# Kernel tuning notes

Hardware: AMD Instinct MI355X
Metric: run time of the kernel (lower is better)

Reference implementation:

```python
import jax, jax.numpy as jnp
import numpy as np
from jax import lax

B, L, W, C, H = 2, 64, 64, 128, 4
DH = C // H  # 32
SCALE = 32 ** -0.5  # dim_head ** -0.5
BN_EPS = 1e-3  # keras BatchNormalization default epsilon


def _sep_conv(x, dwk, dwb, g, b, mu, var, pwk, pwb):
    # Depthwise 3x3 conv, 'same' padding (NHWC, kernel HWIO with groups=C)
    y = lax.conv_general_dilated(
        x, dwk, window_strides=(1, 1), padding='SAME',
        dimension_numbers=('NHWC', 'HWIO', 'NHWC'),
        feature_group_count=x.shape[-1]) + dwb
    # BatchNorm (inference mode: moving statistics)
    y = g * (y - mu) * lax.rsqrt(var + BN_EPS) + b
    # Pointwise 1x1 conv
    return jnp.einsum('blwc,cf->blwf', y, pwk) + pwb


def setup_inputs() -> dict:
    key = jax.random.key(0)
    ks = jax.random.split(key, 32)
    d = {'x': jax.random.normal(ks[0], (B, L * W, C), dtype=jnp.float32)}
    i = 1
    for p in ('q', 'k', 'v'):
        d[p + '_dwk'] = jax.random.normal(ks[i], (3, 3, 1, C), jnp.float32) * 0.1; i += 1
        d[p + '_dwb'] = jax.random.normal(ks[i], (C,), jnp.float32) * 0.05; i += 1
        d[p + '_g'] = jnp.ones((C,), jnp.float32) + jax.random.normal(ks[i], (C,), jnp.float32) * 0.05; i += 1
        d[p + '_b'] = jax.random.normal(ks[i], (C,), jnp.float32) * 0.05; i += 1
        d[p + '_mu'] = jax.random.normal(ks[i], (C,), jnp.float32) * 0.05; i += 1
        d[p + '_var'] = jnp.abs(jax.random.normal(ks[i], (C,), jnp.float32) * 0.1) + 0.9; i += 1
        d[p + '_pwk'] = jax.random.normal(ks[i], (C, C), jnp.float32) * (C ** -0.5); i += 1
        d[p + '_pwb'] = jax.random.normal(ks[i], (C,), jnp.float32) * 0.05; i += 1
    d['out_w'] = jax.random.normal(ks[i], (C, C), jnp.float32) * (C ** -0.5); i += 1
    d['out_b'] = jax.random.normal(ks[i], (C,), jnp.float32) * 0.05
    return d


def reference(x,
              q_dwk, q_dwb, q_g, q_b, q_mu, q_var, q_pwk, q_pwb,
              k_dwk, k_dwb, k_g, k_b, k_mu, k_var, k_pwk, k_pwb,
              v_dwk, v_dwb, v_g, v_b, v_mu, v_var, v_pwk, v_pwb,
              out_w, out_b):
    xi = x.reshape(B, L, W, C)  # 'b (l w) c -> b l w c'
    def heads(t):  # 'b l w (h d) -> b h (l w) d'
        return t.reshape(B, L * W, H, DH).transpose(0, 2, 1, 3)
    q = heads(_sep_conv(xi, q_dwk, q_dwb, q_g, q_b, q_mu, q_var, q_pwk, q_pwb))
    k = heads(_sep_conv(xi, k_dwk, k_dwb, k_g, k_b, k_mu, k_var, k_pwk, k_pwb))
    v = heads(_sep_conv(xi, v_dwk, v_dwb, v_g, v_b, v_mu, v_var, v_pwk, v_pwb))
    dots = jnp.einsum('bhid,bhjd->bhij', q, k) * SCALE
    attn = jax.nn.softmax(dots, axis=-1)
    out = jnp.einsum('bhij,bhjd->bhid', attn, v)
    out = out.transpose(0, 2, 1, 3).reshape(B, L * W, C)  # 'b h c d -> b c (h d)'
    return out @ out_w + out_b  # to_out Dense (dropout is identity at inference)
```

## Files before the change

### kernel.cpp

```cpp
#include <hip/hip_runtime.h>
#include <hip/hip_bf16.h>

#define NN 4096
#define CC 128

typedef __bf16 bf16x8_t __attribute__((ext_vector_type(8)));
typedef __bf16 bf16x4_t __attribute__((ext_vector_type(4)));
typedef float f32x4 __attribute__((ext_vector_type(4)));

static constexpr float SCALE = 0.17677669529663687f;
static constexpr float LOG2E = 1.4426950408889634f;
static constexpr float BN_EPS = 1e-3f;

struct PrecompArgs {
    const float *g[3], *b[3], *mu[3], *var[3], *dwb[3], *pwk[3], *pwb[3];
    float *Wp[3], *bias[3];
};

__global__ __launch_bounds__(128) void precomp_kernel(PrecompArgs A) {
    int q = blockIdx.x;
    int f = threadIdx.x;
    __shared__ float sS[128], sB[128];
    {
        int c = f;
        float rs = rsqrtf(A.var[q][c] + BN_EPS);
        float s = A.g[q][c] * rs;
        sS[c] = s;
        sB[c] = s * (A.dwb[q][c] - A.mu[q][c]) + A.b[q][c];
    }
    __syncthreads();
    float qs = (q == 0) ? SCALE * LOG2E : 1.0f;
    const float* pwk = A.pwk[q];
    float* Wp = A.Wp[q];
    float bias = A.pwb[q][f];
    for (int c = 0; c < 128; ++c) {
        float w = pwk[c * 128 + f];
        Wp[c * 128 + f] = qs * sS[c] * w;
        bias += sB[c] * w;
    }
    A.bias[q][f] = qs * bias;
}

struct ConvArgs {
    const float* x;
    const float* dwk[3];
    const float* Wp[3];
    const float* bias[3];
    __bf16* out[3];
};

__global__ __launch_bounds__(256) void conv_kernel(ConvArgs A) {
    int qkv  = blockIdx.x >> 8;
    int tile = blockIdx.x & 255;
    int b    = tile >> 7;
    int t32  = tile & 127;
    int n0   = t32 * 32;
    int l    = n0 >> 6;
    int w0   = n0 & 63;
    int tid  = threadIdx.x;

    __shared__ float dwl[32][128];

    const float* dwk = A.dwk[qkv];
    {
        int c  = tid & 127;
        int ph = tid >> 7;
        float kd[9];
#pragma unroll
        for (int t = 0; t < 9; ++t) kd[t] = dwk[t * 128 + c];
        float acc[16];
#pragma unroll
        for (int j = 0; j < 16; ++j) acc[j] = 0.f;
        int wbase = w0 + ph * 16;
        const float* xb = A.x + (size_t)b * NN * CC + c;
#pragma unroll
        for (int dl = 0; dl < 3; ++dl) {
            int ll = l + dl - 1;
            if (ll < 0 || ll >= 64) continue;
#pragma unroll
            for (int wx = 0; wx < 18; ++wx) {
                int ww = wbase + wx - 1;
                if (ww < 0 || ww >= 64) continue;
                float xv = xb[(ll * 64 + ww) * 128];
                if (wx < 16)               acc[wx]     += xv * kd[dl * 3 + 0];
                if (wx >= 1 && wx < 17)    acc[wx - 1] += xv * kd[dl * 3 + 1];
                if (wx >= 2)               acc[wx - 2] += xv * kd[dl * 3 + 2];
            }
        }
#pragma unroll
        for (int j = 0; j < 16; ++j) dwl[ph * 16 + j][c] = acc[j];
    }
    __syncthreads();
    {
        int fg = tid & 31;
        int pg = tid >> 5;
        const float* Wp = A.Wp[qkv];
        float a[4][4];
#pragma unroll
        for (int i = 0; i < 4; ++i)
#pragma unroll
            for (int j = 0; j < 4; ++j) a[i][j] = 0.f;
        for (int c = 0; c < 128; ++c) {
            f32x4 wv = *(const f32x4*)&Wp[c * 128 + fg * 4];
#pragma unroll
            for (int i = 0; i < 4; ++i) {
                float d = dwl[pg * 4 + i][c];
                a[i][0] += d * wv[0];
                a[i][1] += d * wv[1];
                a[i][2] += d * wv[2];
                a[i][3] += d * wv[3];
            }
        }
        f32x4 bs = *(const f32x4*)&A.bias[qkv][fg * 4];
        int f0 = fg * 4;
        int h  = f0 >> 5;
        int dh0 = f0 & 31;
        __bf16* dst = A.out[qkv] + ((size_t)(b * 4 + h) * NN) * 32 + dh0;
#pragma unroll
        for (int i = 0; i < 4; ++i) {
            int n = n0 + pg * 4 + i;
            bf16x4_t v;
            v[0] = (__bf16)(a[i][0] + bs[0]);
            v[1] = (__bf16)(a[i][1] + bs[1]);
            v[2] = (__bf16)(a[i][2] + bs[2]);
            v[3] = (__bf16)(a[i][3] + bs[3]);
            *(bf16x4_t*)(dst + (size_t)n * 32) = v;
        }
    }
}

__global__ __launch_bounds__(256, 2) void attn_kernel(
        const __bf16* __restrict__ qg, const __bf16* __restrict__ kg,
        const __bf16* __restrict__ vg, float* __restrict__ Og) {
    int bid = blockIdx.x;
    int bh  = bid & 7;
    int qt  = bid >> 3;
    int b   = bh >> 2, h = bh & 3;
    int tid = threadIdx.x;
    int wv  = tid >> 6;
    int lane = tid & 63;
    int lg  = lane >> 4;
    int lr  = lane & 15;

    __shared__ __bf16 Kl[2][64][40];
    __shared__ __bf16 Vt[2][32][68];

    const __bf16* Kbh = kg + (size_t)bh * NN * 32;
    const __bf16* Vbh = vg + (size_t)bh * NN * 32;

    int qrow0 = qt * 64 + wv * 16;
    bf16x8_t Qf = *(const bf16x8_t*)(qg + ((size_t)bh * NN + qrow0 + lr) * 32 + lg * 8);

    f32x4 acc0 = {0.f, 0.f, 0.f, 0.f};
    f32x4 acc1 = {0.f, 0.f, 0.f, 0.f};
    f32x4 zero4 = {0.f, 0.f, 0.f, 0.f};
    float mr = -1e30f, lsum = 0.f;

    int skey = tid >> 2;
    int sdh8 = (tid & 3) * 8;

    {
        uint4 kk = *(const uint4*)(Kbh + (size_t)skey * 32 + sdh8);
        uint4 vv = *(const uint4*)(Vbh + (size_t)skey * 32 + sdh8);
        *(uint4*)&Kl[0][skey][sdh8] = kk;
        const __bf16* vp = (const __bf16*)&vv;
#pragma unroll
        for (int j = 0; j < 8; ++j) Vt[0][sdh8 + j][skey] = vp[j];
    }
    __syncthreads();

    uint4 kk, vv;
    for (int t = 0; t < 64; ++t) {
        int cur = t & 1;
        if (t < 63) {
            int k0n = (t + 1) * 64;
            kk = *(const uint4*)(Kbh + (size_t)(k0n + skey) * 32 + sdh8);
            vv = *(const uint4*)(Vbh + (size_t)(k0n + skey) * 32 + sdh8);
        }
        f32x4 s[4];
#pragma unroll
        for (int kb = 0; kb < 4; ++kb) {
            bf16x8_t Kf = *(const bf16x8_t*)&Kl[cur][kb * 16 + lr][lg * 8];
            s[kb] = __builtin_amdgcn_mfma_f32_16x16x32_bf16(Kf, Qf, zero4, 0, 0, 0);
        }
        float tm = -1e30f;
#pragma unroll
        for (int kb = 0; kb < 4; ++kb)
#pragma unroll
            for (int r = 0; r < 4; ++r) tm = fmaxf(tm, s[kb][r]);
        tm = fmaxf(tm, __shfl_xor(tm, 16));
        tm = fmaxf(tm, __shfl_xor(tm, 32));
        float mnew = fmaxf(mr, tm);
        float alpha = exp2f(mr - mnew);
        mr = mnew;
        float p[16];
        float rsum = 0.f;
#pragma unroll
        for (int kb = 0; kb < 4; ++kb)
#pragma unroll
            for (int r = 0; r < 4; ++r) {
                float pv = exp2f(s[kb][r] - mnew);
                p[kb * 4 + r] = pv;
                rsum += pv;
            }
        rsum += __shfl_xor(rsum, 16);
        rsum += __shfl_xor(rsum, 32);
        lsum = lsum * alpha + rsum;
#pragma unroll
        for (int r = 0; r < 4; ++r) {
            float ao = __shfl(alpha, lg * 4 + r);
            acc0[r] *= ao;
            acc1[r] *= ao;
        }
        bf16x8_t PA0, PA1;
#pragma unroll
        for (int j = 0; j < 8; ++j) {
            PA0[j] = (__bf16)p[j];
            PA1[j] = (__bf16)p[8 + j];
        }
#pragma unroll
        for (int m = 0; m < 2; ++m) {
            bf16x8_t Pf = (m == 0) ? PA0 : PA1;
            bf16x4_t a0 = *(const bf16x4_t*)&Vt[cur][lr][32 * m + 4 * lg];
            bf16x4_t a1 = *(const bf16x4_t*)&Vt[cur][lr][32 * m + 16 + 4 * lg];
            bf16x8_t B0;
#pragma unroll
            for (int j = 0; j < 4; ++j) { B0[j] = a0[j]; B0[4 + j] = a1[j]; }
            acc0 = __builtin_amdgcn_mfma_f32_16x16x32_bf16(Pf, B0, acc0, 0, 0, 0);
            bf16x4_t c0 = *(const bf16x4_t*)&Vt[cur][lr + 16][32 * m + 4 * lg];
            bf16x4_t c1 = *(const bf16x4_t*)&Vt[cur][lr + 16][32 * m + 16 + 4 * lg];
            bf16x8_t B1;
#pragma unroll
            for (int j = 0; j < 4; ++j) { B1[j] = c0[j]; B1[4 + j] = c1[j]; }
            acc1 = __builtin_amdgcn_mfma_f32_16x16x32_bf16(Pf, B1, acc1, 0, 0, 0);
        }
        if (t < 63) {
            *(uint4*)&Kl[cur ^ 1][skey][sdh8] = kk;
            const __bf16* vp = (const __bf16*)&vv;
#pragma unroll
            for (int j = 0; j < 8; ++j) Vt[cur ^ 1][sdh8 + j][skey] = vp[j];
        }
        __syncthreads();
    }

    float* ob = Og + (size_t)b * NN * 128 + (size_t)h * 32;
    int nrow = qrow0 + lg * 4;
#pragma unroll
    for (int r = 0; r < 4; ++r) {
        float inv = 1.f / __shfl(lsum, lg * 4 + r);
        ob[(size_t)(nrow + r) * 128 + lr]      = acc0[r] * inv;
        ob[(size_t)(nrow + r) * 128 + lr + 16] = acc1[r] * inv;
    }
}

__global__ __launch_bounds__(256) void outproj_kernel(
        const float* __restrict__ Og, const float* __restrict__ ow,
        const float* __restrict__ obias, float* __restrict__ out) {
    int tile = blockIdx.x;
    int b = tile >> 7, t32 = tile & 127;
    int n0 = t32 * 32;
    int tid = threadIdx.x;
    __shared__ float Ol[32][128];
#pragma unroll
    for (int r2 = 0; r2 < 16; ++r2) {
        int idx = r2 * 256 + tid;
        int p = idx >> 7, c = idx & 127;
        Ol[p][c] = Og[((size_t)b * NN + n0 + p) * 128 + c];
    }
    __syncthreads();
    int fg = tid & 31, pg = tid >> 5;
    float a[4][4];
#pragma unroll
    for (int i = 0; i < 4; ++i)
#pragma unroll
        for (int j = 0; j < 4; ++j) a[i][j] = 0.f;
    for (int c = 0; c < 128; ++c) {
        f32x4 wv4 = *(const f32x4*)&ow[c * 128 + fg * 4];
#pragma unroll
        for (int i = 0; i < 4; ++i) {
            float d = Ol[pg * 4 + i][c];
            a[i][0] += d * wv4[0];
            a[i][1] += d * wv4[1];
            a[i][2] += d * wv4[2];
            a[i][3] += d * wv4[3];
        }
    }
    f32x4 bs = *(const f32x4*)&obias[fg * 4];
#pragma unroll
    for (int i = 0; i < 4; ++i) {
        int n = n0 + pg * 4 + i;
        f32x4 v;
        v[0] = a[i][0] + bs[0];
        v[1] = a[i][1] + bs[1];
        v[2] = a[i][2] + bs[2];
        v[3] = a[i][3] + bs[3];
        *(f32x4*)(out + ((size_t)b * NN + n) * 128 + fg * 4) = v;
    }
}

extern "C" void kernel_launch(void* const* d_in, const int* in_sizes, int n_in,
                              void* d_out, int out_size, void* d_ws, size_t ws_size,
                              hipStream_t stream) {
    const float* x = (const float*)d_in[0];
    char* ws = (char*)d_ws;

    float* Wp[3];
    float* biasp[3];
    __bf16* qkvp[3];
    for (int i = 0; i < 3; ++i) {
        Wp[i]    = (float*)(ws + (size_t)i * 65536);
        biasp[i] = (float*)(ws + 196608 + (size_t)i * 512);
        qkvp[i]  = (__bf16*)(ws + 262144 + (size_t)i * 2097152);
    }
    float* O = (float*)(ws + 262144 + 3 * (size_t)2097152);

    PrecompArgs pa;
    ConvArgs ca;
    ca.x = x;
    for (int i = 0; i < 3; ++i) {
        int base = 1 + 8 * i;
        ca.dwk[i] = (const float*)d_in[base + 0];
        pa.dwb[i] = (const float*)d_in[base + 1];
        pa.g[i]   = (const float*)d_in[base + 2];
        pa.b[i]   = (const float*)d_in[base + 3];
        pa.mu[i]  = (const float*)d_in[base + 4];
        pa.var[i] = (const float*)d_in[base + 5];
        pa.pwk[i] = (const float*)d_in[base + 6];
        pa.pwb[i] = (const float*)d_in[base + 7];
        pa.Wp[i] = Wp[i];
        pa.bias[i] = biasp[i];
        ca.Wp[i] = Wp[i];
        ca.bias[i] = biasp[i];
        ca.out[i] = qkvp[i];
    }

    hipLaunchKernelGGL(precomp_kernel, dim3(3), dim3(128), 0, stream, pa);
    hipLaunchKernelGGL(conv_kernel, dim3(768), dim3(256), 0, stream, ca);
    hipLaunchKernelGGL(attn_kernel, dim3(512), dim3(256), 0, stream,
                       qkvp[0], qkvp[1], qkvp[2], O);
    hipLaunchKernelGGL(outproj_kernel, dim3(256), dim3(256), 0, stream,
                       O, (const float*)d_in[25], (const float*)d_in[26],
                       (float*)d_out);
}
```

Before: 293.8 us.

## Split attention keys across waves, load K to registers, lazy rescale

Each attention block now handles 32 query rows, and the key range is split in half between wave pairs, a split-K flash attention. The two partial softmax states are merged through shared memory at the end, and the grid doubles to 1024 blocks. K fragments are loaded straight from global memory into registers instead of going through LDS. Online-softmax rescaling is skipped unless the running max grows by more than a threshold. This targets occupancy, LDS traffic and exp/shuffle work, at the cost of more registers, a final merge step, and bf16 probabilities that can reach values up to 2^8.

```diff
diff --git a/kernel.cpp b/kernel.cpp
--- a/kernel.cpp
+++ b/kernel.cpp
@@ -129,7 +129,7 @@
     }
 }
 
-__global__ __launch_bounds__(256, 2) void attn_kernel(
+__global__ __launch_bounds__(256, 4) void attn_kernel(
         const __bf16* __restrict__ qg, const __bf16* __restrict__ kg,
         const __bf16* __restrict__ vg, float* __restrict__ Og) {
     int bid = blockIdx.x;
@@ -141,48 +141,59 @@
     int lane = tid & 63;
     int lg  = lane >> 4;
     int lr  = lane & 15;
-
-    __shared__ __bf16 Kl[2][64][40];
-    __shared__ __bf16 Vt[2][32][68];
+    int qsub  = wv & 1;
+    int khalf = wv >> 1;
+
+    __shared__ __bf16 Vt[2][2][32][68];
 
     const __bf16* Kbh = kg + (size_t)bh * NN * 32;
     const __bf16* Vbh = vg + (size_t)bh * NN * 32;
 
-    int qrow0 = qt * 64 + wv * 16;
+    int qrow0 = qt * 32 + qsub * 16;
     bf16x8_t Qf = *(const bf16x8_t*)(qg + ((size_t)bh * NN + qrow0 + lr) * 32 + lg * 8);
+    const __bf16* Kw = Kbh + (size_t)khalf * 2048 * 32;
 
     f32x4 acc0 = {0.f, 0.f, 0.f, 0.f};
     f32x4 acc1 = {0.f, 0.f, 0.f, 0.f};
     f32x4 zero4 = {0.f, 0.f, 0.f, 0.f};
     float mr = -1e30f, lsum = 0.f;
 
-    int skey = tid >> 2;
-    int sdh8 = (tid & 3) * 8;
+    int shalf = tid >> 7;
+    int st    = tid & 127;
+    int skey  = st >> 1;
+    int sdh   = (st & 1) * 16;
+    const __bf16* Vw = Vbh + (size_t)shalf * 2048 * 32;
 
     {
-        uint4 kk = *(const uint4*)(Kbh + (size_t)skey * 32 + sdh8);
-        uint4 vv = *(const uint4*)(Vbh + (size_t)skey * 32 + sdh8);
-        *(uint4*)&Kl[0][skey][sdh8] = kk;
-        const __bf16* vp = (const __bf16*)&vv;
-#pragma unroll
-        for (int j = 0; j < 8; ++j) Vt[0][sdh8 + j][skey] = vp[j];
-    }
-    __syncthreads();
-
-    uint4 kk, vv;
-    for (int t = 0; t < 64; ++t) {
+        bf16x8_t v0 = *(const bf16x8_t*)(Vw + (size_t)skey * 32 + sdh);
+        bf16x8_t v1 = *(const bf16x8_t*)(Vw + (size_t)skey * 32 + sdh + 8);
+#pragma unroll
+        for (int j = 0; j < 8; ++j) {
+            Vt[0][shalf][sdh + j][skey]     = v0[j];
+            Vt[0][shalf][sdh + 8 + j][skey] = v1[j];
+        }
+    }
+    bf16x8_t kf[4], kfn[4];
+#pragma unroll
+    for (int kb = 0; kb < 4; ++kb)
+        kf[kb] = *(const bf16x8_t*)(Kw + (size_t)(kb * 16 + lr) * 32 + lg * 8);
+    __syncthreads();
+
+    bf16x8_t vv0, vv1;
+    for (int t = 0; t < 32; ++t) {
         int cur = t & 1;
-        if (t < 63) {
+        if (t < 31) {
             int k0n = (t + 1) * 64;
-            kk = *(const uint4*)(Kbh + (size_t)(k0n + skey) * 32 + sdh8);
-            vv = *(const uint4*)(Vbh + (size_t)(k0n + skey) * 32 + sdh8);
+            vv0 = *(const bf16x8_t*)(Vw + (size_t)(k0n + skey) * 32 + sdh);
+            vv1 = *(const bf16x8_t*)(Vw + (size_t)(k0n + skey) * 32 + sdh + 8);
+#pragma unroll
+            for (int kb = 0; kb < 4; ++kb)
+                kfn[kb] = *(const bf16x8_t*)(Kw + (size_t)(k0n + kb * 16 + lr) * 32 + lg * 8);
         }
         f32x4 s[4];
 #pragma unroll
-        for (int kb = 0; kb < 4; ++kb) {
-            bf16x8_t Kf = *(const bf16x8_t*)&Kl[cur][kb * 16 + lr][lg * 8];
-            s[kb] = __builtin_amdgcn_mfma_f32_16x16x32_bf16(Kf, Qf, zero4, 0, 0, 0);
-        }
+        for (int kb = 0; kb < 4; ++kb)
+            s[kb] = __builtin_amdgcn_mfma_f32_16x16x32_bf16(kf[kb], Qf, zero4, 0, 0, 0);
         float tm = -1e30f;
 #pragma unroll
         for (int kb = 0; kb < 4; ++kb)
@@ -190,9 +201,8 @@
             for (int r = 0; r < 4; ++r) tm = fmaxf(tm, s[kb][r]);
         tm = fmaxf(tm, __shfl_xor(tm, 16));
         tm = fmaxf(tm, __shfl_xor(tm, 32));
-        float mnew = fmaxf(mr, tm);
-        float alpha = exp2f(mr - mnew);
-        mr = mnew;
+        bool need = __any(tm > mr + 8.0f);
+        float mnew = need ? fmaxf(mr, tm) : mr;
         float p[16];
         float rsum = 0.f;
 #pragma unroll
@@ -205,12 +215,18 @@
             }
         rsum += __shfl_xor(rsum, 16);
         rsum += __shfl_xor(rsum, 32);
-        lsum = lsum * alpha + rsum;
-#pragma unroll
-        for (int r = 0; r < 4; ++r) {
-            float ao = __shfl(alpha, lg * 4 + r);
-            acc0[r] *= ao;
-            acc1[r] *= ao;
+        if (need) {
+            float alpha = exp2f(mr - mnew);
+            lsum = lsum * alpha + rsum;
+#pragma unroll
+            for (int r = 0; r < 4; ++r) {
+                float ao = __shfl(alpha, lg * 4 + r);
+                acc0[r] *= ao;
+                acc1[r] *= ao;
+            }
+            mr = mnew;
+        } else {
+            lsum += rsum;
         }
         bf16x8_t PA0, PA1;
 #pragma unroll
@@ -221,35 +237,61 @@
 #pragma unroll
         for (int m = 0; m < 2; ++m) {
             bf16x8_t Pf = (m == 0) ? PA0 : PA1;
-            bf16x4_t a0 = *(const bf16x4_t*)&Vt[cur][lr][32 * m + 4 * lg];
-            bf16x4_t a1 = *(const bf16x4_t*)&Vt[cur][lr][32 * m + 16 + 4 * lg];
+            bf16x4_t a0 = *(const bf16x4_t*)&Vt[cur][khalf][lr][32 * m + 4 * lg];
+            bf16x4_t a1 = *(const bf16x4_t*)&Vt[cur][khalf][lr][32 * m + 16 + 4 * lg];
             bf16x8_t B0;
 #pragma unroll
             for (int j = 0; j < 4; ++j) { B0[j] = a0[j]; B0[4 + j] = a1[j]; }
             acc0 = __builtin_amdgcn_mfma_f32_16x16x32_bf16(Pf, B0, acc0, 0, 0, 0);
-            bf16x4_t c0 = *(const bf16x4_t*)&Vt[cur][lr + 16][32 * m + 4 * lg];
-            bf16x4_t c1 = *(const bf16x4_t*)&Vt[cur][lr + 16][32 * m + 16 + 4 * lg];
+            bf16x4_t c0 = *(const bf16x4_t*)&Vt[cur][khalf][lr + 16][32 * m + 4 * lg];
+            bf16x4_t c1 = *(const bf16x4_t*)&Vt[cur][khalf][lr + 16][32 * m + 16 + 4 * lg];
             bf16x8_t B1;
 #pragma unroll
             for (int j = 0; j < 4; ++j) { B1[j] = c0[j]; B1[4 + j] = c1[j]; }
             acc1 = __builtin_amdgcn_mfma_f32_16x16x32_bf16(Pf, B1, acc1, 0, 0, 0);
         }
-        if (t < 63) {
-            *(uint4*)&Kl[cur ^ 1][skey][sdh8] = kk;
-            const __bf16* vp = (const __bf16*)&vv;
-#pragma unroll
-            for (int j = 0; j < 8; ++j) Vt[cur ^ 1][sdh8 + j][skey] = vp[j];
+        if (t < 31) {
+#pragma unroll
+            for (int j = 0; j < 8; ++j) {
+                Vt[cur ^ 1][shalf][sdh + j][skey]     = vv0[j];
+                Vt[cur ^ 1][shalf][sdh + 8 + j][skey] = vv1[j];
+            }
+#pragma unroll
+            for (int kb = 0; kb < 4; ++kb) kf[kb] = kfn[kb];
         }
         __syncthreads();
     }
 
-    float* ob = Og + (size_t)b * NN * 128 + (size_t)h * 32;
-    int nrow = qrow0 + lg * 4;
-#pragma unroll
-    for (int r = 0; r < 4; ++r) {
-        float inv = 1.f / __shfl(lsum, lg * 4 + r);
-        ob[(size_t)(nrow + r) * 128 + lr]      = acc0[r] * inv;
-        ob[(size_t)(nrow + r) * 128 + lr + 16] = acc1[r] * inv;
+    float* mrg = (float*)&Vt[0][0][0][0];
+    if (wv >= 2) {
+        float* d = mrg + ((wv - 2) * 64 + lane) * 12;
+#pragma unroll
+        for (int r = 0; r < 4; ++r) { d[r] = acc0[r]; d[4 + r] = acc1[r]; }
+        d[8] = mr; d[9] = lsum;
+    }
+    __syncthreads();
+    if (wv < 2) {
+        const float* d = mrg + (wv * 64 + lane) * 12;
+        f32x4 pacc0, pacc1;
+#pragma unroll
+        for (int r = 0; r < 4; ++r) { pacc0[r] = d[r]; pacc1[r] = d[4 + r]; }
+        float pm = d[8], pl = d[9];
+        float m  = fmaxf(mr, pm);
+        float a  = exp2f(mr - m);
+        float pa = exp2f(pm - m);
+        float l  = lsum * a + pl * pa;
+        float* ob = Og + (size_t)b * NN * 128 + (size_t)h * 32;
+        int nrow = qrow0 + lg * 4;
+#pragma unroll
+        for (int r = 0; r < 4; ++r) {
+            float ar  = __shfl(a,  lg * 4 + r);
+            float par = __shfl(pa, lg * 4 + r);
+            float inv = 1.f / __shfl(l, lg * 4 + r);
+            float o0 = acc0[r] * ar + pacc0[r] * par;
+            float o1 = acc1[r] * ar + pacc1[r] * par;
+            ob[(size_t)(nrow + r) * 128 + lr]      = o0 * inv;
+            ob[(size_t)(nrow + r) * 128 + lr + 16] = o1 * inv;
+        }
     }
 }
 
@@ -336,7 +378,7 @@
 
     hipLaunchKernelGGL(precomp_kernel, dim3(3), dim3(128), 0, stream, pa);
     hipLaunchKernelGGL(conv_kernel, dim3(768), dim3(256), 0, stream, ca);
-    hipLaunchKernelGGL(attn_kernel, dim3(512), dim3(256), 0, stream,
+    hipLaunchKernelGGL(attn_kernel, dim3(1024), dim3(256), 0, stream,
                        qkvp[0], qkvp[1], qkvp[2], O);
     hipLaunchKernelGGL(outproj_kernel, dim3(256), dim3(256), 0, stream,
                        O, (const float*)d_in[25], (const float*)d_in[26],
```

Result: faster. 277.3 us (-5.6%).
